# Performance work log

Measured on AMD Instinct MI355X. Metric: run time of the kernel, lower is better.

The kernel has to match this reference:

```python
import jax, jax.numpy as jnp
import numpy as np

EPS = 1e-12  # F.normalize default eps


def _l2_normalize(x):
    n = jnp.linalg.norm(x, axis=-1, keepdims=True)
    return x / jnp.maximum(n, EPS)


def setup_inputs() -> dict:
    key = jax.random.key(0)
    k1, k2 = jax.random.split(key)
    B, N, D = 2048, 100000, 256
    query = jax.random.normal(k1, (B, D), dtype=jnp.float32)
    memory_states = jax.random.normal(k2, (N, D), dtype=jnp.float32)
    return {"query": query, "memory_states": memory_states, "k": 8}


def reference(query, memory_states, k):
    # cosine-similarity retrieval: normalize both sides, dense matmul, top-k, gather
    mem_norm = _l2_normalize(memory_states)          # [N, D]
    query_norm = _l2_normalize(query)                # [B, D]
    scores = query_norm @ mem_norm.T                 # [B, N]
    top_k_scores, indices = jax.lax.top_k(scores, k)  # [B, k] each
    retrieved = memory_states[indices]               # [B, k, D] (raw, un-normalized states as in torch)
    return retrieved, top_k_scores
```

## Files before the change

kernel.cpp:

```cpp
#include <hip/hip_runtime.h>
#include <hip/hip_bf16.h>
#include <stdint.h>

#define DIM 256
#define TOPK 8
#define NSTRIPS 64
#define STRIP_TOP 8
#define QT 256
#define NT 64
#define CAND (NSTRIPS * STRIP_TOP)
#define RESCORE 64
#define SLOTS 33
#define IDXMASK 0x1FFFFu

typedef __attribute__((ext_vector_type(8))) short short8;
typedef __attribute__((ext_vector_type(4))) float floatx4;
typedef __attribute__((address_space(3))) unsigned int lds_u32;
typedef __attribute__((address_space(1))) const unsigned int gbl_u32;

__device__ __forceinline__ unsigned short f2bf(float f) {
    union { float f; uint32_t u; } v; v.f = f;
    uint32_t u = v.u;
    uint32_t r = u + 0x7fffu + ((u >> 16) & 1u);
    return (unsigned short)(r >> 16);
}

__device__ __forceinline__ uint32_t umaxu(uint32_t a, uint32_t b) { return a > b ? a : b; }
__device__ __forceinline__ uint32_t uminu(uint32_t a, uint32_t b) { return a < b ? a : b; }

__device__ __forceinline__ void top8_insert(uint32_t* ts, uint32_t key) {
#pragma unroll
    for (int j = 0; j < STRIP_TOP - 1; j++) {
        uint32_t m;
        asm("v_med3_u32 %0, %1, %2, %3" : "=v"(m) : "v"(ts[j]), "v"(ts[j + 1]), "v"(key));
        ts[j] = m;
    }
    ts[STRIP_TOP - 1] = umaxu(ts[STRIP_TOP - 1], key);
}

__global__ void prep_kernel(const float* __restrict__ query,
                            const float* __restrict__ mem,
                            float* __restrict__ rnorm_mem,
                            unsigned short* __restrict__ q_bf16,
                            unsigned short* __restrict__ mem_bf16,
                            int B, int N)
{
    int wave = threadIdx.x >> 6;
    int lane = threadIdx.x & 63;
    int row  = blockIdx.x * 4 + wave;
    int total = N + B;
    if (row >= total) return;
    const float* src = (row < N) ? (mem + (size_t)row * DIM)
                                 : (query + (size_t)(row - N) * DIM);
    float4 v = ((const float4*)src)[lane];
    float ss = v.x * v.x + v.y * v.y + v.z * v.z + v.w * v.w;
#pragma unroll
    for (int m = 32; m >= 1; m >>= 1) ss += __shfl_xor(ss, m, 64);
    float rinv = 1.0f / fmaxf(sqrtf(ss), 1e-12f);
    ushort4 o;
    o.x = f2bf(v.x * rinv); o.y = f2bf(v.y * rinv);
    o.z = f2bf(v.z * rinv); o.w = f2bf(v.w * rinv);
    if (row < N) {
        if (lane == 0) rnorm_mem[row] = rinv;
        if (mem_bf16) ((ushort4*)(mem_bf16 + (size_t)row * DIM))[lane] = o;
    } else {
        ((ushort4*)(q_bf16 + (size_t)(row - N) * DIM))[lane] = o;
    }
}

template<bool PRE>
__global__ __launch_bounds__(512, 4) void score_select_kernel(
    const float* __restrict__ mem,
    const float* __restrict__ rnorm_mem,
    const unsigned short* __restrict__ mem_bf16,
    const unsigned short* __restrict__ q_bf16,
    uint32_t* __restrict__ cand_key,
    int B, int N)
{
    __shared__ unsigned short lds_m[NT * DIM];
    __shared__ uint32_t lds_s[QT * SLOTS];

    const int t    = threadIdx.x;
    const int wave = t >> 6;
    const int lane = t & 63;
    const int quad = lane >> 4;
    const int l16  = lane & 15;

    const int lin  = (int)(blockIdx.x + gridDim.x * blockIdx.y);
    const int SPX  = NSTRIPS / 8;
    const int strip = (lin & 7) * SPX + ((lin >> 3) % SPX);
    const int qb    = (lin >> 3) / SPX;
    const int qbase = qb * QT;

    const int SS    = (N + NSTRIPS - 1) / NSTRIPS;
    const int n0    = strip * SS;
    const int nend  = (n0 + SS < N) ? (n0 + SS) : N;
    const int limit = nend - n0;
    const int ntiles = (limit + NT - 1) / NT;

    short8 afrag[2][8];
#pragma unroll
    for (int s = 0; s < 2; s++) {
        int qrow = qbase + s * 128 + wave * 16 + l16;
        const unsigned short* qp = q_bf16 + (size_t)qrow * DIM + quad * 8;
#pragma unroll
        for (int ks = 0; ks < 8; ks++)
            afrag[s][ks] = *(const short8*)(qp + ks * 32);
    }

    uint32_t ts[STRIP_TOP];
#pragma unroll
    for (int j = 0; j < STRIP_TOP; j++) ts[j] = 0;

    const int l5  = lane >> 5;
    const int s32 = lane & 31;

    auto stage = [&](int tileIdx) {
        int base = n0 + tileIdx * NT;
        if (PRE) {
#pragma unroll
            for (int is = 0; is < 4; is++) {
                int rl = is * 16 + wave * 2 + l5;
                int n = base + rl; if (n >= nend) n = nend - 1;
                int chunk = s32 ^ (rl & 7);
                const unsigned short* gp = mem_bf16 + (size_t)n * DIM + chunk * 8;
                unsigned short* lp = lds_m + (is * 16 + wave * 2) * DIM;
                __builtin_amdgcn_global_load_lds((gbl_u32*)(const void*)gp,
                                                 (lds_u32*)(void*)lp, 16, 0, 0);
            }
        } else {
#pragma unroll 4
            for (int i = 0; i < 8; i++) {
                int rl = i * 8 + wave;
                int n = base + rl;
                ushort4 o;
                if (n < nend) {
                    float rinv = rnorm_mem[n];
                    float4 v = ((const float4*)(mem + (size_t)n * DIM))[lane];
                    o.x = f2bf(v.x * rinv); o.y = f2bf(v.y * rinv);
                    o.z = f2bf(v.z * rinv); o.w = f2bf(v.w * rinv);
                } else { o.x = 0; o.y = 0; o.z = 0; o.w = 0; }
                int slot = (lane >> 1) ^ (rl & 7);
                *(ushort4*)(lds_m + rl * DIM + slot * 8 + (lane & 1) * 4) = o;
            }
        }
    };

    stage(0);
    __syncthreads();

    const int qloc = t & 255;
    const int half = t >> 8;

    const floatx4 one4 = {1.f, 1.f, 1.f, 1.f};
    for (int tile = 0; tile < ntiles; tile++) {
        floatx4 acc[2][4];
#pragma unroll
        for (int s = 0; s < 2; s++)
#pragma unroll
            for (int nt = 0; nt < 4; nt++) acc[s][nt] = one4;

#pragma unroll
        for (int ks = 0; ks < 8; ks++) {
#pragma unroll
            for (int nt = 0; nt < 4; nt++) {
                int row = nt * 16 + l16;
                int slot = (ks * 4 + quad) ^ (l16 & 7);
                short8 b = *(const short8*)(lds_m + row * DIM + slot * 8);
#pragma unroll
                for (int s = 0; s < 2; s++)
                    acc[s][nt] = __builtin_amdgcn_mfma_f32_16x16x32_bf16(afrag[s][ks], b, acc[s][nt], 0, 0, 0);
            }
        }
#pragma unroll
        for (int s = 0; s < 2; s++) {
            int qrow = s * 128 + wave * 16 + quad * 4;
#pragma unroll
            for (int r = 0; r < 4; r++) {
                uint32_t u0 = __float_as_uint(fmaxf(acc[s][0][r], 0.f));
                uint32_t u1 = __float_as_uint(fmaxf(acc[s][1][r], 0.f));
                uint32_t u2 = __float_as_uint(fmaxf(acc[s][2][r], 0.f));
                uint32_t u3 = __float_as_uint(fmaxf(acc[s][3][r], 0.f));
                lds_s[(qrow + r) * SLOTS + l16]      = (u2 & 0xFFFF0000u) | (u0 >> 16);
                lds_s[(qrow + r) * SLOTS + 16 + l16] = (u3 & 0xFFFF0000u) | (u1 >> 16);
            }
        }
        __syncthreads();

        if (tile + 1 < ntiles) stage(tile + 1);

        const int tloc = tile * NT;
        const uint4* sp = (const uint4*)(lds_s + (size_t)qloc * SLOTS + half * 16);
        bool full = (tloc + NT <= limit);
#pragma unroll
        for (int j4 = 0; j4 < 4; j4++) {
            uint4 v4 = sp[j4];
#pragma unroll
            for (int e = 0; e < 4; e++) {
                uint32_t v = (e == 0) ? v4.x : (e == 1) ? v4.y : (e == 2) ? v4.z : v4.w;
                int j = half * 16 + j4 * 4 + e;
                uint32_t key_lo = (v << 16) | (uint32_t)(tloc + j);
                uint32_t key_hi = (v & 0xFFFF0000u) | (uint32_t)(tloc + j + 32);
                if (!full) {
                    if (tloc + j >= limit)      key_lo = 0;
                    if (tloc + j + 32 >= limit) key_hi = 0;
                }
                uint32_t kmax = umaxu(key_lo, key_hi);
                uint32_t kmin = uminu(key_lo, key_hi);
                if (__any(kmax > ts[0])) {
                    top8_insert(ts, kmax);
                    if (__any(kmin > ts[0]))
                        top8_insert(ts, kmin);
                }
            }
        }
        __syncthreads();
    }

    if (half) {
#pragma unroll
        for (int j = 0; j < STRIP_TOP; j++) lds_s[qloc * SLOTS + j] = ts[j];
    }
    __syncthreads();
    if (!half) {
#pragma unroll
        for (int j = 0; j < STRIP_TOP; j++)
            top8_insert(ts, lds_s[qloc * SLOTS + j]);

        size_t off = ((size_t)(qbase + qloc) * NSTRIPS + strip) * STRIP_TOP;
#pragma unroll
        for (int j = 0; j < STRIP_TOP; j++) {
            uint32_t k = ts[j];
            uint32_t loc = k & 0xFFFFu;
            uint32_t key2 = ((k >> 17) << 17) | (uint32_t)(n0 + (int)loc);
            cand_key[off + j] = key2;
        }
    }
}

__global__ __launch_bounds__(256) void rescore_kernel(
    const float* __restrict__ query,
    const float* __restrict__ mem,
    const uint32_t* __restrict__ cand_key,
    float* __restrict__ out,
    int B, int N)
{
    __shared__ uint32_t cs[CAND];
    __shared__ float  lds_q[DIM];
    __shared__ double red[4];
    __shared__ double qss_sh;
    __shared__ int    sel_i[RESCORE];
    __shared__ double rs[RESCORE];
    __shared__ double best_s[TOPK];
    __shared__ int    best_i[TOPK];

    const int t    = threadIdx.x;
    const int q    = blockIdx.x;
    const int lane = t & 63;
    const int wave = t >> 6;

    for (int i = t; i < CAND; i += 256)
        cs[i] = cand_key[(size_t)q * CAND + i];

    float qv = query[(size_t)q * DIM + t];
    lds_q[t] = qv;
    double p = (double)qv * (double)qv;
#pragma unroll
    for (int m = 32; m >= 1; m >>= 1) p += __shfl_xor(p, m, 64);
    if (lane == 0) red[wave] = p;
    __syncthreads();
    if (t == 0) qss_sh = red[0] + red[1] + red[2] + red[3];

    {
        uint32_t* qcs = cs + wave * 128;
        for (int k = 2; k <= 128; k <<= 1) {
            for (int j = k >> 1; j > 0; j >>= 1) {
                int i  = 2 * lane - (lane & (j - 1));
                int ip = i + j;
                bool up = ((i & k) == 0);
                uint32_t a = qcs[i], b2 = qcs[ip];
                bool aFirst = a > b2;
                bool doSwap = up ? (!aFirst) : aFirst;
                if (doSwap) { qcs[i] = b2; qcs[ip] = a; }
            }
        }
        if (lane < 16) sel_i[wave * 16 + lane] = (int)(qcs[lane] & IDXMASK);
    }
    __syncthreads();

    double qss = qss_sh;
    for (int r = 0; r < 16; r++) {
        int c = wave * 16 + r;
        int idx = sel_i[c];
        float4 mv = ((const float4*)(mem + (size_t)idx * DIM))[lane];
        float4 qv4 = ((const float4*)lds_q)[lane];
        double dqm = (double)mv.x * (double)qv4.x + (double)mv.y * (double)qv4.y
                   + (double)mv.z * (double)qv4.z + (double)mv.w * (double)qv4.w;
        double dmm = (double)mv.x * (double)mv.x + (double)mv.y * (double)mv.y
                   + (double)mv.z * (double)mv.z + (double)mv.w * (double)mv.w;
#pragma unroll
        for (int m = 32; m >= 1; m >>= 1) {
            dqm += __shfl_xor(dqm, m, 64);
            dmm += __shfl_xor(dmm, m, 64);
        }
        if (lane == 0)
            rs[c] = dqm / (fmax(sqrt(qss), 1e-12) * fmax(sqrt(dmm), 1e-12));
    }
    __syncthreads();

    if (t == 0) {
        double bs[TOPK]; int bi[TOPK];
        for (int i = 0; i < TOPK; i++) { bs[i] = -1e300; bi[i] = 0x7fffffff; }
        for (int c = 0; c < RESCORE; c++) {
            double s = rs[c]; int id = sel_i[c];
            bool better = (s > bs[TOPK - 1]) || (s == bs[TOPK - 1] && id < bi[TOPK - 1]);
            if (better) {
                int pos = TOPK - 1;
                while (pos > 0) {
                    bool b2 = (s > bs[pos - 1]) || (s == bs[pos - 1] && id < bi[pos - 1]);
                    if (!b2) break;
                    bs[pos] = bs[pos - 1]; bi[pos] = bi[pos - 1]; pos--;
                }
                bs[pos] = s; bi[pos] = id;
            }
        }
        for (int i = 0; i < TOPK; i++) { best_s[i] = bs[i]; best_i[i] = bi[i]; }
    }
    __syncthreads();

    size_t score_base = (size_t)B * TOPK * DIM;
    if (t < TOPK) out[score_base + (size_t)q * TOPK + t] = (float)best_s[t];

#pragma unroll
    for (int rep = 0; rep < 2; rep++) {
        int j  = t >> 5;
        int d4 = (t & 31) + rep * 32;
        int idx = best_i[j];
        float4 v = ((const float4*)(mem + (size_t)idx * DIM))[d4];
        ((float4*)(out + ((size_t)q * TOPK + j) * DIM))[d4] = v;
    }
}

extern "C" void kernel_launch(void* const* d_in, const int* in_sizes, int n_in,
                              void* d_out, int out_size, void* d_ws, size_t ws_size,
                              hipStream_t stream)
{
    const float* query = (const float*)d_in[0];
    const float* mem   = (const float*)d_in[1];
    int B = in_sizes[0] / DIM;
    int N = in_sizes[1] / DIM;

    auto align256 = [](size_t x) { return (x + 255) & ~(size_t)255; };
    size_t off = 0;
    auto alloc = [&](size_t bytes) { void* p = (char*)d_ws + off; off += align256(bytes); return p; };

    float* rnorm_mem       = (float*)alloc((size_t)N * 4);
    unsigned short* q_bf16 = (unsigned short*)alloc((size_t)B * DIM * 2);
    uint32_t* cand_key     = (uint32_t*)alloc((size_t)B * CAND * 4);
    size_t base_need = off;
    unsigned short* mem_bf16 = (unsigned short*)((char*)d_ws + base_need);
    bool pre = (base_need + align256((size_t)N * DIM * 2)) <= ws_size;
    if (!pre) mem_bf16 = nullptr;

    int prep_blocks = (N + B + 3) / 4;
    prep_kernel<<<prep_blocks, 256, 0, stream>>>(query, mem, rnorm_mem, q_bf16,
                                                 mem_bf16, B, N);

    dim3 g2((B + QT - 1) / QT, NSTRIPS);
    if (pre)
        score_select_kernel<true><<<g2, 512, 0, stream>>>(mem, rnorm_mem, mem_bf16, q_bf16,
                                                          cand_key, B, N);
    else
        score_select_kernel<false><<<g2, 512, 0, stream>>>(mem, rnorm_mem, mem_bf16, q_bf16,
                                                           cand_key, B, N);

    rescore_kernel<<<B, 256, 0, stream>>>(query, mem, cand_key, (float*)d_out, B, N);
}
```

Before: 399.6 us.

## Keep top-k in MFMA registers and double-buffer memory tiles

Swaps the MFMA operand roles so each lane holds scores for one query column directly in its accumulators. It then does the per-lane top-8 insertion straight from registers, removing the LDS score-transpose buffer. The memory tile is double-buffered so the next tile's load is issued before the current tile's MFMAs, dropping one barrier per tile, and a final LDS merge combines the four per-quad partial lists. The trade-off is more registers (two top-8 lists per lane) and an unconditional insert of every score, since the wave-level __any early-out was dropped, which adds VALU work per tile.

New measurement: 430.7 us. +7.8%, slower.

```diff
diff --git a/kernel.cpp b/kernel.cpp
--- a/kernel.cpp
+++ b/kernel.cpp
@@ -10,7 +10,6 @@
 #define NT 64
 #define CAND (NSTRIPS * STRIP_TOP)
 #define RESCORE 64
-#define SLOTS 33
 #define IDXMASK 0x1FFFFu
 
 typedef __attribute__((ext_vector_type(8))) short short8;
@@ -26,7 +25,6 @@
 }
 
 __device__ __forceinline__ uint32_t umaxu(uint32_t a, uint32_t b) { return a > b ? a : b; }
-__device__ __forceinline__ uint32_t uminu(uint32_t a, uint32_t b) { return a < b ? a : b; }
 
 __device__ __forceinline__ void top8_insert(uint32_t* ts, uint32_t key) {
 #pragma unroll
@@ -77,8 +75,7 @@
     uint32_t* __restrict__ cand_key,
     int B, int N)
 {
-    __shared__ unsigned short lds_m[NT * DIM];
-    __shared__ uint32_t lds_s[QT * SLOTS];
+    __shared__ unsigned short lds_m[2][NT * DIM];
 
     const int t    = threadIdx.x;
     const int wave = t >> 6;
@@ -98,24 +95,26 @@
     const int limit = nend - n0;
     const int ntiles = (limit + NT - 1) / NT;
 
-    short8 afrag[2][8];
-#pragma unroll
-    for (int s = 0; s < 2; s++) {
-        int qrow = qbase + s * 128 + wave * 16 + l16;
+    short8 qfrag[2][8];
+#pragma unroll
+    for (int b = 0; b < 2; b++) {
+        int qrow = qbase + wave * 32 + b * 16 + l16;
         const unsigned short* qp = q_bf16 + (size_t)qrow * DIM + quad * 8;
 #pragma unroll
         for (int ks = 0; ks < 8; ks++)
-            afrag[s][ks] = *(const short8*)(qp + ks * 32);
-    }
-
-    uint32_t ts[STRIP_TOP];
-#pragma unroll
-    for (int j = 0; j < STRIP_TOP; j++) ts[j] = 0;
+            qfrag[b][ks] = *(const short8*)(qp + ks * 32);
+    }
+
+    uint32_t ts[2][STRIP_TOP];
+#pragma unroll
+    for (int b = 0; b < 2; b++)
+#pragma unroll
+        for (int j = 0; j < STRIP_TOP; j++) ts[b][j] = 0;
 
     const int l5  = lane >> 5;
     const int s32 = lane & 31;
 
-    auto stage = [&](int tileIdx) {
+    auto stage = [&](unsigned short* lbase, int tileIdx) {
         int base = n0 + tileIdx * NT;
         if (PRE) {
 #pragma unroll
@@ -124,7 +123,7 @@
                 int n = base + rl; if (n >= nend) n = nend - 1;
                 int chunk = s32 ^ (rl & 7);
                 const unsigned short* gp = mem_bf16 + (size_t)n * DIM + chunk * 8;
-                unsigned short* lp = lds_m + (is * 16 + wave * 2) * DIM;
+                unsigned short* lp = lbase + (is * 16 + wave * 2) * DIM;
                 __builtin_amdgcn_global_load_lds((gbl_u32*)(const void*)gp,
                                                  (lds_u32*)(void*)lp, 16, 0, 0);
             }
@@ -141,98 +140,92 @@
                     o.z = f2bf(v.z * rinv); o.w = f2bf(v.w * rinv);
                 } else { o.x = 0; o.y = 0; o.z = 0; o.w = 0; }
                 int slot = (lane >> 1) ^ (rl & 7);
-                *(ushort4*)(lds_m + rl * DIM + slot * 8 + (lane & 1) * 4) = o;
+                *(ushort4*)(lbase + rl * DIM + slot * 8 + (lane & 1) * 4) = o;
             }
         }
     };
 
-    stage(0);
-    __syncthreads();
-
-    const int qloc = t & 255;
-    const int half = t >> 8;
+    stage(&lds_m[0][0], 0);
+    __syncthreads();
 
     const floatx4 one4 = {1.f, 1.f, 1.f, 1.f};
     for (int tile = 0; tile < ntiles; tile++) {
-        floatx4 acc[2][4];
-#pragma unroll
-        for (int s = 0; s < 2; s++)
-#pragma unroll
-            for (int nt = 0; nt < 4; nt++) acc[s][nt] = one4;
+        unsigned short* lbuf = &lds_m[tile & 1][0];
+        if (tile + 1 < ntiles) stage(&lds_m[(tile + 1) & 1][0], tile + 1);
+
+        floatx4 acc[4][2];
+#pragma unroll
+        for (int a = 0; a < 4; a++)
+#pragma unroll
+            for (int b = 0; b < 2; b++) acc[a][b] = one4;
 
 #pragma unroll
         for (int ks = 0; ks < 8; ks++) {
 #pragma unroll
-            for (int nt = 0; nt < 4; nt++) {
-                int row = nt * 16 + l16;
+            for (int a = 0; a < 4; a++) {
+                int row = a * 16 + l16;
                 int slot = (ks * 4 + quad) ^ (l16 & 7);
-                short8 b = *(const short8*)(lds_m + row * DIM + slot * 8);
-#pragma unroll
-                for (int s = 0; s < 2; s++)
-                    acc[s][nt] = __builtin_amdgcn_mfma_f32_16x16x32_bf16(afrag[s][ks], b, acc[s][nt], 0, 0, 0);
-            }
-        }
-#pragma unroll
-        for (int s = 0; s < 2; s++) {
-            int qrow = s * 128 + wave * 16 + quad * 4;
-#pragma unroll
-            for (int r = 0; r < 4; r++) {
-                uint32_t u0 = __float_as_uint(fmaxf(acc[s][0][r], 0.f));
-                uint32_t u1 = __float_as_uint(fmaxf(acc[s][1][r], 0.f));
-                uint32_t u2 = __float_as_uint(fmaxf(acc[s][2][r], 0.f));
-                uint32_t u3 = __float_as_uint(fmaxf(acc[s][3][r], 0.f));
-                lds_s[(qrow + r) * SLOTS + l16]      = (u2 & 0xFFFF0000u) | (u0 >> 16);
-                lds_s[(qrow + r) * SLOTS + 16 + l16] = (u3 & 0xFFFF0000u) | (u1 >> 16);
-            }
-        }
+                short8 m = *(const short8*)(lbuf + row * DIM + slot * 8);
+#pragma unroll
+                for (int b = 0; b < 2; b++)
+                    acc[a][b] = __builtin_amdgcn_mfma_f32_16x16x32_bf16(m, qfrag[b][ks], acc[a][b], 0, 0, 0);
+            }
+        }
+
+        const int tb0 = tile * NT + quad * 4;
+        const bool full = (tile * NT + NT <= limit);
+        if (full) {
+#pragma unroll
+            for (int b = 0; b < 2; b++)
+#pragma unroll
+                for (int a = 0; a < 4; a++)
+#pragma unroll
+                    for (int r = 0; r < 4; r++) {
+                        uint32_t u = __float_as_uint(fmaxf(acc[a][b][r], 0.f));
+                        uint32_t key = (u & 0xFFFF0000u) | (uint32_t)(tb0 + a * 16 + r);
+                        top8_insert(ts[b], key);
+                    }
+        } else {
+#pragma unroll
+            for (int b = 0; b < 2; b++)
+#pragma unroll
+                for (int a = 0; a < 4; a++)
+#pragma unroll
+                    for (int r = 0; r < 4; r++) {
+                        int loc = tb0 + a * 16 + r;
+                        uint32_t u = __float_as_uint(fmaxf(acc[a][b][r], 0.f));
+                        uint32_t key = (u & 0xFFFF0000u) | (uint32_t)loc;
+                        if (loc >= limit) key = 0;
+                        top8_insert(ts[b], key);
+                    }
+        }
+
         __syncthreads();
-
-        if (tile + 1 < ntiles) stage(tile + 1);
-
-        const int tloc = tile * NT;
-        const uint4* sp = (const uint4*)(lds_s + (size_t)qloc * SLOTS + half * 16);
-        bool full = (tloc + NT <= limit);
-#pragma unroll
-        for (int j4 = 0; j4 < 4; j4++) {
-            uint4 v4 = sp[j4];
-#pragma unroll
-            for (int e = 0; e < 4; e++) {
-                uint32_t v = (e == 0) ? v4.x : (e == 1) ? v4.y : (e == 2) ? v4.z : v4.w;
-                int j = half * 16 + j4 * 4 + e;
-                uint32_t key_lo = (v << 16) | (uint32_t)(tloc + j);
-                uint32_t key_hi = (v & 0xFFFF0000u) | (uint32_t)(tloc + j + 32);
-                if (!full) {
-                    if (tloc + j >= limit)      key_lo = 0;
-                    if (tloc + j + 32 >= limit) key_hi = 0;
-                }
-                uint32_t kmax = umaxu(key_lo, key_hi);
-                uint32_t kmin = uminu(key_lo, key_hi);
-                if (__any(kmax > ts[0])) {
-                    top8_insert(ts, kmax);
-                    if (__any(kmin > ts[0]))
-                        top8_insert(ts, kmin);
-                }
-            }
-        }
-        __syncthreads();
-    }
-
-    if (half) {
-#pragma unroll
-        for (int j = 0; j < STRIP_TOP; j++) lds_s[qloc * SLOTS + j] = ts[j];
-    }
-    __syncthreads();
-    if (!half) {
+    }
+
+    uint32_t* sc = (uint32_t*)&lds_m[0][0];
+#pragma unroll
+    for (int b = 0; b < 2; b++)
 #pragma unroll
         for (int j = 0; j < STRIP_TOP; j++)
-            top8_insert(ts, lds_s[qloc * SLOTS + j]);
-
-        size_t off = ((size_t)(qbase + qloc) * NSTRIPS + strip) * STRIP_TOP;
+            sc[((wave * 32 + b * 16 + l16) * 4 + quad) * 9 + j] = ts[b][j];
+    __syncthreads();
+
+    if (t < QT) {
+        uint32_t best[STRIP_TOP];
+#pragma unroll
+        for (int j = 0; j < STRIP_TOP; j++) best[j] = sc[(t * 4 + 0) * 9 + j];
+#pragma unroll
+        for (int qd = 1; qd < 4; qd++)
+#pragma unroll
+            for (int j = 0; j < STRIP_TOP; j++)
+                top8_insert(best, sc[(t * 4 + qd) * 9 + j]);
+
+        size_t off = ((size_t)(qbase + t) * NSTRIPS + strip) * STRIP_TOP;
 #pragma unroll
         for (int j = 0; j < STRIP_TOP; j++) {
-            uint32_t k = ts[j];
-            uint32_t loc = k & 0xFFFFu;
-            uint32_t key2 = ((k >> 17) << 17) | (uint32_t)(n0 + (int)loc);
+            uint32_t k = best[j];
+            uint32_t key2 = ((k >> 17) << 17) | (uint32_t)(n0 + (int)(k & 0xFFFFu));
             cand_key[off + j] = key2;
         }
     }
```
